# Kernel tuning notes

Hardware: AMD Instinct MI355X
Metric: run time of the kernel (lower is better)

Reference implementation:

```python
import jax, jax.numpy as jnp
import numpy as np

DIM = 16
N_HEADS = 4
HEAD_DIM = DIM // N_HEADS
B = 2097152


def setup_inputs() -> dict:
    key = jax.random.key(0)
    k1, k2, k3, k4, k5, k6 = jax.random.split(key, 6)
    return {
        "fp_16": jax.random.normal(k1, (B, DIM), dtype=jnp.float32),
        "chem_16": jax.random.normal(k2, (B, DIM), dtype=jnp.float32),
        "in_proj_weight": jax.random.normal(k3, (3 * DIM, DIM), dtype=jnp.float32) * 0.25,
        "in_proj_bias": jax.random.normal(k4, (3 * DIM,), dtype=jnp.float32) * 0.02,
        "out_proj_weight": jax.random.normal(k5, (DIM, DIM), dtype=jnp.float32) * 0.25,
        "out_proj_bias": jax.random.normal(k6, (DIM,), dtype=jnp.float32) * 0.02,
    }


def reference(fp_16, chem_16, in_proj_weight, in_proj_bias, out_proj_weight, out_proj_bias):
    # nn.MultiheadAttention packed QKV projection split
    Wq, Wk, Wv = in_proj_weight[:DIM], in_proj_weight[DIM:2 * DIM], in_proj_weight[2 * DIM:]
    bq, bk, bv = in_proj_bias[:DIM], in_proj_bias[DIM:2 * DIM], in_proj_bias[2 * DIM:]

    q = fp_16 @ Wq.T + bq      # (B, 16)
    k = chem_16 @ Wk.T + bk    # (B, 16)
    v = chem_16 @ Wv.T + bv    # (B, 16)

    # Single-token attention: seq_len_q = seq_len_kv = 1.
    # Per-head scores (B, H, 1, 1); softmax over a length-1 key axis is exactly 1,
    # so attn_out == v. Computed explicitly for faithfulness (cheap at this scale).
    qh = q.reshape(B, N_HEADS, HEAD_DIM)
    kh = k.reshape(B, N_HEADS, HEAD_DIM)
    vh = v.reshape(B, N_HEADS, HEAD_DIM)
    scores = jnp.einsum("bhd,bhd->bh", qh, kh) / jnp.sqrt(jnp.float32(HEAD_DIM))
    w = jax.nn.softmax(scores[..., None], axis=-1)  # (B, H, 1) -> all ones
    attn = (w * vh.reshape(B, N_HEADS, 1, HEAD_DIM).squeeze(2)[..., None, :].squeeze(-2)[..., None] * 0 + vh) if False else w[..., 0:1] * vh  # (B, H, hd)
    attn = attn.reshape(B, DIM)

    return attn @ out_proj_weight.T + out_proj_bias  # (B, 16)
```

## Files before the change

### kernel.cpp

```cpp
#include <hip/hip_runtime.h>


#define DIM 16
#define BATCH 2097152

__global__ void fold_weights_kernel(const float* __restrict__ in_proj_weight,
                                    const float* __restrict__ in_proj_bias,
                                    const float* __restrict__ out_proj_weight,
                                    const float* __restrict__ out_proj_bias,
                                    float* __restrict__ ws) {
    int t = threadIdx.x;
    int j = t >> 4;
    int i = t & 15;
    float acc = 0.0f;
#pragma unroll
    for (int k = 0; k < 16; ++k)
        acc += out_proj_weight[j * 16 + k] * in_proj_weight[(32 + k) * 16 + i];
    ws[t] = acc;
    if (t < 16) {
        float b = out_proj_bias[t];
#pragma unroll
        for (int k = 0; k < 16; ++k)
            b += out_proj_weight[t * 16 + k] * in_proj_bias[32 + k];
        ws[256 + t] = b;
    }
}

__global__ __launch_bounds__(256) void affine_rows_kernel(
    const float* __restrict__ x,
    const float* __restrict__ wfold,
    float* __restrict__ out) {
    size_t row = (size_t)blockIdx.x * 256 + threadIdx.x;
    if (row >= (size_t)BATCH) return;

    const float4* xv = (const float4*)(x + row * DIM);
    float4 x0 = xv[0];
    float4 x1 = xv[1];
    float4 x2 = xv[2];
    float4 x3 = xv[3];
    float xr[16] = {x0.x, x0.y, x0.z, x0.w,
                    x1.x, x1.y, x1.z, x1.w,
                    x2.x, x2.y, x2.z, x2.w,
                    x3.x, x3.y, x3.z, x3.w};

    float acc[16];
#pragma unroll
    for (int j = 0; j < 16; ++j)
        acc[j] = wfold[256 + j];
#pragma unroll
    for (int j = 0; j < 16; ++j) {
#pragma unroll
        for (int i = 0; i < 16; ++i)
            acc[j] += xr[i] * wfold[j * 16 + i];
    }

    float4* ov = (float4*)(out + row * DIM);
    ov[0] = make_float4(acc[0],  acc[1],  acc[2],  acc[3]);
    ov[1] = make_float4(acc[4],  acc[5],  acc[6],  acc[7]);
    ov[2] = make_float4(acc[8],  acc[9],  acc[10], acc[11]);
    ov[3] = make_float4(acc[12], acc[13], acc[14], acc[15]);
}

extern "C" void kernel_launch(void* const* d_in, const int* in_sizes, int n_in,
                              void* d_out, int out_size, void* d_ws, size_t ws_size,
                              hipStream_t stream) {
    const float* chem        = (const float*)d_in[1];
    const float* in_proj_w   = (const float*)d_in[2];
    const float* in_proj_b   = (const float*)d_in[3];
    const float* out_proj_w  = (const float*)d_in[4];
    const float* out_proj_b  = (const float*)d_in[5];
    float* out = (float*)d_out;
    float* ws  = (float*)d_ws;

    fold_weights_kernel<<<1, 256, 0, stream>>>(in_proj_w, in_proj_b,
                                               out_proj_w, out_proj_b, ws);

    int blocks = BATCH / 256;
    affine_rows_kernel<<<blocks, 256, 0, stream>>>(chem, ws, out);
}
```

Baseline: 297.4 us.

## Map four lanes per row with coalesced float4 loads and quad shuffles

```diff
diff --git a/kernel.cpp b/kernel.cpp
--- a/kernel.cpp
+++ b/kernel.cpp
@@ -26,39 +26,62 @@
     }
 }
 
-__global__ __launch_bounds__(256) void affine_rows_kernel(
+__device__ __forceinline__ float4 shfl_xor_f4(float4 v, int mask) {
+    float4 r;
+    r.x = __shfl_xor(v.x, mask, 64);
+    r.y = __shfl_xor(v.y, mask, 64);
+    r.z = __shfl_xor(v.z, mask, 64);
+    r.w = __shfl_xor(v.w, mask, 64);
+    return r;
+}
+
+__global__ __launch_bounds__(256) void affine_rows_coalesced(
     const float* __restrict__ x,
     const float* __restrict__ wfold,
     float* __restrict__ out) {
-    size_t row = (size_t)blockIdx.x * 256 + threadIdx.x;
-    if (row >= (size_t)BATCH) return;
+    const int t = threadIdx.x;
+    const int q = t & 3;
 
-    const float4* xv = (const float4*)(x + row * DIM);
-    float4 x0 = xv[0];
-    float4 x1 = xv[1];
-    float4 x2 = xv[2];
-    float4 x3 = xv[3];
-    float xr[16] = {x0.x, x0.y, x0.z, x0.w,
-                    x1.x, x1.y, x1.z, x1.w,
-                    x2.x, x2.y, x2.z, x2.w,
-                    x3.x, x3.y, x3.z, x3.w};
+    float4 w[4][4];
+#pragma unroll
+    for (int m = 0; m < 4; ++m) {
+        const int qc = q ^ m;
+#pragma unroll
+        for (int jp = 0; jp < 4; ++jp)
+            w[m][jp] = *(const float4*)(wfold + (q * 4 + jp) * 16 + qc * 4);
+    }
+    const float4 bias = *(const float4*)(wfold + 256 + q * 4);
 
-    float acc[16];
+    const float4* xv = (const float4*)x;
+    float4* ov = (float4*)out;
+    const size_t base = (size_t)blockIdx.x * 1024;
+
 #pragma unroll
-    for (int j = 0; j < 16; ++j)
-        acc[j] = wfold[256 + j];
-#pragma unroll
-    for (int j = 0; j < 16; ++j) {
-#pragma unroll
-        for (int i = 0; i < 16; ++i)
-            acc[j] += xr[i] * wfold[j * 16 + i];
+    for (int k = 0; k < 4; ++k) {
+        const size_t idx = base + (size_t)k * 256 + t;
+        float4 xs0 = xv[idx];
+        float4 xs1 = shfl_xor_f4(xs0, 1);
+        float4 xs2 = shfl_xor_f4(xs0, 2);
+        float4 xs3 = shfl_xor_f4(xs0, 3);
+
+        float4 acc = bias;
+#define ACCUM(m, xsv)                                                   \
+        acc.x += xsv.x * w[m][0].x + xsv.y * w[m][0].y +                \
+                 xsv.z * w[m][0].z + xsv.w * w[m][0].w;                 \
+        acc.y += xsv.x * w[m][1].x + xsv.y * w[m][1].y +                \
+                 xsv.z * w[m][1].z + xsv.w * w[m][1].w;                 \
+        acc.z += xsv.x * w[m][2].x + xsv.y * w[m][2].y +                \
+                 xsv.z * w[m][2].z + xsv.w * w[m][2].w;                 \
+        acc.w += xsv.x * w[m][3].x + xsv.y * w[m][3].y +                \
+                 xsv.z * w[m][3].z + xsv.w * w[m][3].w;
+        ACCUM(0, xs0)
+        ACCUM(1, xs1)
+        ACCUM(2, xs2)
+        ACCUM(3, xs3)
+#undef ACCUM
+
+        ov[idx] = acc;
     }
-
-    float4* ov = (float4*)(out + row * DIM);
-    ov[0] = make_float4(acc[0],  acc[1],  acc[2],  acc[3]);
-    ov[1] = make_float4(acc[4],  acc[5],  acc[6],  acc[7]);
-    ov[2] = make_float4(acc[8],  acc[9],  acc[10], acc[11]);
-    ov[3] = make_float4(acc[12], acc[13], acc[14], acc[15]);
 }
 
 extern "C" void kernel_launch(void* const* d_in, const int* in_sizes, int n_in,
@@ -75,6 +98,6 @@
     fold_weights_kernel<<<1, 256, 0, stream>>>(in_proj_w, in_proj_b,
                                                out_proj_w, out_proj_b, ws);
 
-    int blocks = BATCH / 256;
-    affine_rows_kernel<<<blocks, 256, 0, stream>>>(chem, ws, out);
+    const int blocks = BATCH / 256;
+    affine_rows_coalesced<<<blocks, 256, 0, stream>>>(chem, ws, out);
 }
```

Result: faster. 285.9 us (-3.8%).
